# Optimization experiments

Hardware: AMD Instinct MI355X
Metric: run time of the kernel (lower is better)

The kernel has to match this reference:

```python
import jax, jax.numpy as jnp
import numpy as np

N = 100000      # nodes
E = 3200000     # edges (avg degree 32)
F = 256         # input features
C = 256         # output channels


def setup_inputs() -> dict:
    key = jax.random.key(0)
    k1, k2, k3, k4, k5 = jax.random.split(key, 5)
    x = jax.random.normal(k1, (N, F), dtype=jnp.float32)
    edge_row = jax.random.randint(k2, (E,), 0, N, dtype=jnp.int32)
    edge_col = jax.random.randint(k3, (E,), 0, N, dtype=jnp.int32)
    # precomputed normalized adjacency values (D^-1/2 (A+I) D^-1/2 entries)
    edge_vals = jax.random.uniform(k4, (E,), dtype=jnp.float32)
    kernel = jax.random.normal(k5, (F, C), dtype=jnp.float32) * (1.0 / np.sqrt(F))
    bias = jnp.zeros((C,), dtype=jnp.float32)
    return {"x": x, "edge_row": edge_row, "edge_col": edge_col,
            "edge_vals": edge_vals, "kernel": kernel, "bias": bias}


def reference(x, edge_row, edge_col, edge_vals, kernel, bias):
    # GraphConv: Z = relu( A_hat @ (X @ W) + b ), single mode, sparse A_hat.
    h = x @ kernel                                   # [N, C]
    msgs = edge_vals[:, None] * h[edge_col]          # [E, C] gather along cols
    agg = jax.ops.segment_sum(msgs, edge_row, num_segments=N)  # [N, C]
    return jax.nn.relu(agg + bias)
```

## Files before the change

kernel.cpp:

```cpp
#include <hip/hip_runtime.h>
#include <hip/hip_bf16.h>
#include <hip/hip_fp16.h>


#define BROWS 128
#define NBMAX 1024
#define CH_A1 16384
#define CH_A3 8192
#define GEMM_SMEM 10240

typedef __attribute__((ext_vector_type(4))) float f32x4;
typedef __attribute__((ext_vector_type(8))) short s16x8;

__device__ __forceinline__ unsigned short f2bf(float f) {
    unsigned u = __float_as_uint(f);
    u += 0x7FFFu + ((u >> 16) & 1u);
    return (unsigned short)(u >> 16);
}
__device__ __forceinline__ float bf2f(unsigned short s) {
    return __uint_as_float(((unsigned)s) << 16);
}

__global__ __launch_bounds__(256) void kA1h(const int* __restrict__ row,
                                            int* __restrict__ gcnt,
                                            const float* __restrict__ W,
                                            unsigned short* __restrict__ Wt,
                                            int E, int NB, int nHist) {
    __shared__ int h[NBMAX];
    int bid = blockIdx.x;
    int t = threadIdx.x;
    if (bid >= nHist) {
        int idx = (bid - nHist) * 256 + t;
        int k = idx >> 8, c = idx & 255;
        Wt[c * 256 + k] = f2bf(W[idx]);
        return;
    }
    for (int j = t; j < NB; j += 256) h[j] = 0;
    __syncthreads();
    int start = bid * CH_A1;
    int end = min(E, start + CH_A1);
    for (int i = start + t; i < end; i += 256)
        atomicAdd(&h[row[i] >> 7], 1);
    __syncthreads();
    for (int j = t; j < NB; j += 256)
        if (h[j]) atomicAdd(&gcnt[j], h[j]);
}

__global__ __launch_bounds__(1024) void kA2(const int* __restrict__ gcnt,
                                            int* __restrict__ bkt_base,
                                            int* __restrict__ gcur,
                                            int* __restrict__ rowptr,
                                            int NB, int N, int E) {
    __shared__ int s[1024];
    int t = threadIdx.x;
    int v = (t < NB) ? gcnt[t] : 0;
    s[t] = v;
    __syncthreads();
    for (int off = 1; off < 1024; off <<= 1) {
        int tmp = (t >= off) ? s[t - off] : 0;
        __syncthreads();
        if (t >= off) s[t] += tmp;
        __syncthreads();
    }
    if (t < NB) {
        int ex = s[t] - v;
        bkt_base[t] = ex;
        gcur[t] = ex;
    }
    if (t == 0) {
        bkt_base[NB] = E;
        rowptr[N] = E;
    }
}

__device__ __forceinline__ void a3_body(const int* __restrict__ row,
                                        const int* __restrict__ col,
                                        const float* __restrict__ val,
                                        int* __restrict__ gcur,
                                        int2* __restrict__ binned,
                                        int E, int NB, int chunk, char* smem) {
    int* h    = (int*)smem;
    int* base = h + NB;
    int* cur  = base + NB;
    int t = threadIdx.x;
    for (int j = t; j < NB; j += 256) { h[j] = 0; cur[j] = 0; }
    __syncthreads();
    int start = chunk * CH_A3;
    int end = min(E, start + CH_A3);
    for (int i = start + t; i < end; i += 256)
        atomicAdd(&h[row[i] >> 7], 1);
    __syncthreads();
    for (int j = t; j < NB; j += 256) {
        int c = h[j];
        base[j] = c ? atomicAdd(&gcur[j], c) : 0;
    }
    __syncthreads();
    for (int i = start + t; i < end; i += 256) {
        int r = row[i];
        int b = r >> 7;
        int ofs = atomicAdd(&cur[b], 1);
        unsigned hb = (unsigned)__half_as_ushort(__float2half(val[i]));
        binned[base[b] + ofs] = make_int2(col[i] | (int)(hb << 17), r & (BROWS - 1));
    }
}

__device__ __forceinline__ void kb_body(const int2* __restrict__ binned,
                                        const int* __restrict__ bkt_base,
                                        int* __restrict__ rowptr,
                                        unsigned* __restrict__ csr,
                                        int N, int b, char* smem) {
    int* cnt = (int*)smem;
    int* sc  = cnt + BROWS;
    int* cur = sc + BROWS;
    int t = threadIdx.x;
    int r0 = b * BROWS;
    int bb = bkt_base[b];
    int be = bkt_base[b + 1];
    if (t < BROWS) cnt[t] = 0;
    __syncthreads();
    for (int i = bb + t; i < be; i += 256)
        atomicAdd(&cnt[binned[i].y], 1);
    __syncthreads();
    if (t < BROWS) sc[t] = cnt[t];
    __syncthreads();
    for (int off = 1; off < BROWS; off <<= 1) {
        int tmp = (t < BROWS && t >= off) ? sc[t - off] : 0;
        __syncthreads();
        if (t < BROWS && t >= off) sc[t] += tmp;
        __syncthreads();
    }
    if (t < BROWS) {
        int ex = sc[t] - cnt[t];
        cur[t] = ex;
        if (r0 + t < N) rowptr[r0 + t] = bb + ex;
    }
    __syncthreads();
    for (int i = bb + t; i < be; i += 256) {
        int2 e = binned[i];
        int ofs = atomicAdd(&cur[e.y], 1);
        csr[bb + ofs] = (unsigned)e.x;
    }
}

__device__ __forceinline__ void gemm_body(const float* __restrict__ X,
                                          const unsigned short* __restrict__ Wt,
                                          unsigned short* __restrict__ H,
                                          int M, int g, char* smem) {
    typedef unsigned short AsRow[40];
    AsRow* As = (AsRow*)smem;
    int t = threadIdx.x;
    int lane = t & 63;
    int w = t >> 6;
    int wm = w & 1, wn = w >> 1;
    int rb = g >> 2, cb = g & 3;
    int r0 = rb * 128, c0 = cb * 64;

    int srow = t >> 2;
    int sslot = t & 3;
    int gr0 = r0 + srow;        if (gr0 >= M) gr0 = M - 1;
    int gr1 = r0 + 64 + srow;   if (gr1 >= M) gr1 = M - 1;

    f32x4 acc[4][2] = {};

    for (int k0 = 0; k0 < 256; k0 += 32) {
        const float* p0 = &X[(size_t)gr0 * 256 + k0 + sslot * 8];
        const float* p1 = &X[(size_t)gr1 * 256 + k0 + sslot * 8];
        float4 a0 = *(const float4*)p0;
        float4 a1 = *(const float4*)(p0 + 4);
        float4 b0 = *(const float4*)p1;
        float4 b1 = *(const float4*)(p1 + 4);
        s16x8 va, vb;
        va[0] = (short)f2bf(a0.x); va[1] = (short)f2bf(a0.y);
        va[2] = (short)f2bf(a0.z); va[3] = (short)f2bf(a0.w);
        va[4] = (short)f2bf(a1.x); va[5] = (short)f2bf(a1.y);
        va[6] = (short)f2bf(a1.z); va[7] = (short)f2bf(a1.w);
        vb[0] = (short)f2bf(b0.x); vb[1] = (short)f2bf(b0.y);
        vb[2] = (short)f2bf(b0.z); vb[3] = (short)f2bf(b0.w);
        vb[4] = (short)f2bf(b1.x); vb[5] = (short)f2bf(b1.y);
        vb[6] = (short)f2bf(b1.z); vb[7] = (short)f2bf(b1.w);
        __syncthreads();
        *(s16x8*)&As[srow][sslot * 8] = va;
        *(s16x8*)&As[srow + 64][sslot * 8] = vb;
        __syncthreads();

        int kofs = (lane >> 4) * 8;
        s16x8 afr[4], bfr[2];
#pragma unroll
        for (int mi = 0; mi < 4; ++mi)
            afr[mi] = *(const s16x8*)&As[wm * 64 + mi * 16 + (lane & 15)][kofs];
#pragma unroll
        for (int ni = 0; ni < 2; ++ni) {
            int cn = c0 + wn * 32 + ni * 16 + (lane & 15);
            bfr[ni] = *(const s16x8*)&Wt[(size_t)cn * 256 + k0 + kofs];
        }
#pragma unroll
        for (int mi = 0; mi < 4; ++mi)
#pragma unroll
            for (int ni = 0; ni < 2; ++ni)
                acc[mi][ni] = __builtin_amdgcn_mfma_f32_16x16x32_bf16(
                    afr[mi], bfr[ni], acc[mi][ni], 0, 0, 0);
    }

#pragma unroll
    for (int mi = 0; mi < 4; ++mi) {
#pragma unroll
        for (int ni = 0; ni < 2; ++ni) {
            int rg = r0 + wm * 64 + mi * 16 + (lane >> 4) * 4;
            int cg = c0 + wn * 32 + ni * 16 + (lane & 15);
#pragma unroll
            for (int j = 0; j < 4; ++j) {
                if (rg + j < M)
                    H[(size_t)(rg + j) * 256 + cg] = f2bf(acc[mi][ni][j]);
            }
        }
    }
}

__global__ __launch_bounds__(256) void hyb1(const int* __restrict__ row,
                                            const int* __restrict__ col,
                                            const float* __restrict__ val,
                                            int* __restrict__ gcur,
                                            int2* __restrict__ binned,
                                            int E, int NB, int nA3,
                                            const float* __restrict__ X,
                                            const unsigned short* __restrict__ Wt,
                                            unsigned short* __restrict__ H,
                                            int M, int g0) {
    extern __shared__ char smem[];
    int bid = blockIdx.x;
    if (bid < nA3) { a3_body(row, col, val, gcur, binned, E, NB, bid, smem); return; }
    gemm_body(X, Wt, H, M, g0 + (bid - nA3), smem);
}

__global__ __launch_bounds__(256) void hyb2(const int2* __restrict__ binned,
                                            const int* __restrict__ bktb,
                                            int* __restrict__ rowptr,
                                            unsigned* __restrict__ csr,
                                            int N, int NB,
                                            const float* __restrict__ X,
                                            const unsigned short* __restrict__ Wt,
                                            unsigned short* __restrict__ H,
                                            int M, int g0) {
    extern __shared__ char smem[];
    int bid = blockIdx.x;
    if (bid < NB) { kb_body(binned, bktb, rowptr, csr, N, bid, smem); return; }
    gemm_body(X, Wt, H, M, g0 + (bid - NB), smem);
}

__global__ __launch_bounds__(256) void k_gemm_solo(const float* __restrict__ X,
                                                   const unsigned short* __restrict__ Wt,
                                                   unsigned short* __restrict__ H, int M) {
    extern __shared__ char smem[];
    gemm_body(X, Wt, H, M, blockIdx.x, smem);
}

__global__ __launch_bounds__(256) void k_agg(const unsigned short* __restrict__ H,
                                             const int* __restrict__ rowptr,
                                             const unsigned* __restrict__ csr,
                                             const float* __restrict__ bias,
                                             float* __restrict__ out, int n) {
    int wave = threadIdx.x >> 6;
    int lane = threadIdx.x & 63;
    int node = blockIdx.x * 4 + wave;
    if (node >= n) return;
    int s = rowptr[node];
    int e = rowptr[node + 1];
    int h = lane >> 5;
    int cbase = (lane & 31) * 8;

    float a0=0.f,a1=0.f,a2=0.f,a3=0.f,a4=0.f,a5=0.f,a6=0.f,a7=0.f;

#define ACC(K, HV)                                                      \
    {                                                                   \
        float v = __half2float(__ushort_as_half((unsigned short)((K) >> 17))); \
        a0 += v * bf2f((unsigned short)(HV)[0]);                        \
        a1 += v * bf2f((unsigned short)(HV)[1]);                        \
        a2 += v * bf2f((unsigned short)(HV)[2]);                        \
        a3 += v * bf2f((unsigned short)(HV)[3]);                        \
        a4 += v * bf2f((unsigned short)(HV)[4]);                        \
        a5 += v * bf2f((unsigned short)(HV)[5]);                        \
        a6 += v * bf2f((unsigned short)(HV)[6]);                        \
        a7 += v * bf2f((unsigned short)(HV)[7]);                        \
    }

    int i = s;
    for (; i + 7 < e; i += 8) {
        unsigned k0 = csr[i + h];
        unsigned k1 = csr[i + 2 + h];
        unsigned k2 = csr[i + 4 + h];
        unsigned k3 = csr[i + 6 + h];
        s16x8 h0 = *(const s16x8*)&H[(k0 & 0x1FFFFu) * 256 + cbase];
        s16x8 h1 = *(const s16x8*)&H[(k1 & 0x1FFFFu) * 256 + cbase];
        s16x8 h2 = *(const s16x8*)&H[(k2 & 0x1FFFFu) * 256 + cbase];
        s16x8 h3 = *(const s16x8*)&H[(k3 & 0x1FFFFu) * 256 + cbase];
        ACC(k0, h0); ACC(k1, h1); ACC(k2, h2); ACC(k3, h3);
    }
    for (; i + 1 < e; i += 2) {
        unsigned k0 = csr[i + h];
        s16x8 h0 = *(const s16x8*)&H[(k0 & 0x1FFFFu) * 256 + cbase];
        ACC(k0, h0);
    }
    if (i < e) {
        unsigned k0 = csr[i];
        s16x8 h0 = *(const s16x8*)&H[(k0 & 0x1FFFFu) * 256 + cbase];
        float v = h ? 0.f
                    : __half2float(__ushort_as_half((unsigned short)(k0 >> 17)));
        a0 += v * bf2f((unsigned short)h0[0]);
        a1 += v * bf2f((unsigned short)h0[1]);
        a2 += v * bf2f((unsigned short)h0[2]);
        a3 += v * bf2f((unsigned short)h0[3]);
        a4 += v * bf2f((unsigned short)h0[4]);
        a5 += v * bf2f((unsigned short)h0[5]);
        a6 += v * bf2f((unsigned short)h0[6]);
        a7 += v * bf2f((unsigned short)h0[7]);
    }
#undef ACC

    a0 += __shfl_xor(a0, 32); a1 += __shfl_xor(a1, 32);
    a2 += __shfl_xor(a2, 32); a3 += __shfl_xor(a3, 32);
    a4 += __shfl_xor(a4, 32); a5 += __shfl_xor(a5, 32);
    a6 += __shfl_xor(a6, 32); a7 += __shfl_xor(a7, 32);

    float w0 = h ? a4 : a0;
    float w1 = h ? a5 : a1;
    float w2 = h ? a6 : a2;
    float w3 = h ? a7 : a3;
    int cw = cbase + h * 4;
    float4 b4 = *(const float4*)&bias[cw];
    float4 o;
    o.x = fmaxf(w0 + b4.x, 0.f);
    o.y = fmaxf(w1 + b4.y, 0.f);
    o.z = fmaxf(w2 + b4.z, 0.f);
    o.w = fmaxf(w3 + b4.w, 0.f);
    *(float4*)&out[node * 256 + cw] = o;
}

extern "C" void kernel_launch(void* const* d_in, const int* in_sizes, int n_in,
                              void* d_out, int out_size, void* d_ws, size_t ws_size,
                              hipStream_t stream) {
    const float* x     = (const float*)d_in[0];
    const int*   erow  = (const int*)d_in[1];
    const int*   ecol  = (const int*)d_in[2];
    const float* evals = (const float*)d_in[3];
    const float* W     = (const float*)d_in[4];
    const float* bias  = (const float*)d_in[5];
    float* out = (float*)d_out;

    const int C = 256;
    const int N = in_sizes[0] / C;
    const int E = in_sizes[1];
    const int NB = (N + BROWS - 1) / BROWS;

    char* ws = (char*)d_ws;
    size_t off = 0;
    auto carve = [&](size_t bytes) -> void* {
        void* p = ws + off;
        off += (bytes + 255) & ~(size_t)255;
        return p;
    };
    unsigned short* Hbf  = (unsigned short*)carve((size_t)N * C * 2);
    unsigned*       csr  = (unsigned*)carve((size_t)E * 4);
    int*            rowp = (int*)carve((size_t)(N + 1) * 4);
    unsigned short* Wt   = (unsigned short*)carve((size_t)C * 256 * 2);
    int*            gcnt = (int*)carve((size_t)NB * 4);
    int*            gcur = (int*)carve((size_t)NB * 4);
    int*            bktb = (int*)carve((size_t)(NB + 1) * 4);

    bool fused = (off + (size_t)E * 8) <= ws_size;
    int2* binned = fused ? (int2*)carve((size_t)E * 8) : (int2*)Hbf;

    int nHist = (E + CH_A1 - 1) / CH_A1;
    int nA3   = (E + CH_A3 - 1) / CH_A3;
    int nRB   = (N + 127) / 128;
    int gemmBlocks = nRB * 4;
    int G1 = gemmBlocks / 2;
    int G2 = gemmBlocks - G1;

    hipMemsetAsync(gcnt, 0, (size_t)NB * 4, stream);
    kA1h<<<nHist + 256, 256, 0, stream>>>(erow, gcnt, W, Wt, E, NB, nHist);
    kA2<<<1, 1024, 0, stream>>>(gcnt, bktb, gcur, rowp, NB, N, E);

    if (fused) {
        hyb1<<<nA3 + G1, 256, GEMM_SMEM, stream>>>(erow, ecol, evals, gcur, binned,
                                                   E, NB, nA3, x, Wt, Hbf, N, 0);
        hyb2<<<NB + G2, 256, GEMM_SMEM, stream>>>(binned, bktb, rowp, csr, N, NB,
                                                  x, Wt, Hbf, N, G1);
    } else {
        hyb1<<<nA3, 256, GEMM_SMEM, stream>>>(erow, ecol, evals, gcur, binned,
                                              E, NB, nA3, x, Wt, Hbf, N, 0);
        hyb2<<<NB, 256, GEMM_SMEM, stream>>>(binned, bktb, rowp, csr, N, NB,
                                             x, Wt, Hbf, N, 0);
        k_gemm_solo<<<gemmBlocks, 256, GEMM_SMEM, stream>>>(x, Wt, Hbf, N);
    }

    k_agg<<<(N + 3) / 4, 256, 0, stream>>>(Hbf, rowp, csr, bias, out, N);
}
```

Measured before the change: 435.6 us.

## Store H in 16-column blocked layout and aggregate per column block

```diff
diff --git a/kernel.cpp b/kernel.cpp
--- a/kernel.cpp
+++ b/kernel.cpp
@@ -3,7 +3,7 @@
 #include <hip/hip_fp16.h>
 
 
-#define BROWS 128
+#define BROWS 256
 #define NBMAX 1024
 #define CH_A1 16384
 #define CH_A3 8192
@@ -40,7 +40,7 @@
     int start = bid * CH_A1;
     int end = min(E, start + CH_A1);
     for (int i = start + t; i < end; i += 256)
-        atomicAdd(&h[row[i] >> 7], 1);
+        atomicAdd(&h[row[i] >> 8], 1);
     __syncthreads();
     for (int j = t; j < NB; j += 256)
         if (h[j]) atomicAdd(&gcnt[j], h[j]);
@@ -88,7 +88,7 @@
     int start = chunk * CH_A3;
     int end = min(E, start + CH_A3);
     for (int i = start + t; i < end; i += 256)
-        atomicAdd(&h[row[i] >> 7], 1);
+        atomicAdd(&h[row[i] >> 8], 1);
     __syncthreads();
     for (int j = t; j < NB; j += 256) {
         int c = h[j];
@@ -97,7 +97,7 @@
     __syncthreads();
     for (int i = start + t; i < end; i += 256) {
         int r = row[i];
-        int b = r >> 7;
+        int b = r >> 8;
         int ofs = atomicAdd(&cur[b], 1);
         unsigned hb = (unsigned)__half_as_ushort(__float2half(val[i]));
         binned[base[b] + ofs] = make_int2(col[i] | (int)(hb << 17), r & (BROWS - 1));
@@ -116,24 +116,23 @@
     int r0 = b * BROWS;
     int bb = bkt_base[b];
     int be = bkt_base[b + 1];
-    if (t < BROWS) cnt[t] = 0;
+    cnt[t] = 0;
     __syncthreads();
     for (int i = bb + t; i < be; i += 256)
         atomicAdd(&cnt[binned[i].y], 1);
     __syncthreads();
-    if (t < BROWS) sc[t] = cnt[t];
-    __syncthreads();
-    for (int off = 1; off < BROWS; off <<= 1) {
-        int tmp = (t < BROWS && t >= off) ? sc[t - off] : 0;
-        __syncthreads();
-        if (t < BROWS && t >= off) sc[t] += tmp;
-        __syncthreads();
-    }
-    if (t < BROWS) {
-        int ex = sc[t] - cnt[t];
-        cur[t] = ex;
-        if (r0 + t < N) rowptr[r0 + t] = bb + ex;
-    }
+    int v = cnt[t];
+    sc[t] = v;
+    __syncthreads();
+    for (int off = 1; off < 256; off <<= 1) {
+        int tmp = (t >= off) ? sc[t - off] : 0;
+        __syncthreads();
+        if (t >= off) sc[t] += tmp;
+        __syncthreads();
+    }
+    int ex = sc[t] - v;
+    cur[t] = ex;
+    if (r0 + t < N) rowptr[r0 + t] = bb + ex;
     __syncthreads();
     for (int i = bb + t; i < be; i += 256) {
         int2 e = binned[i];
@@ -144,7 +143,7 @@
 
 __device__ __forceinline__ void gemm_body(const float* __restrict__ X,
                                           const unsigned short* __restrict__ Wt,
-                                          unsigned short* __restrict__ H,
+                                          unsigned short* __restrict__ Hb,
                                           int M, int g, char* smem) {
     typedef unsigned short AsRow[40];
     AsRow* As = (AsRow*)smem;
@@ -152,8 +151,8 @@
     int lane = t & 63;
     int w = t >> 6;
     int wm = w & 1, wn = w >> 1;
-    int rb = g >> 2, cb = g & 3;
-    int r0 = rb * 128, c0 = cb * 64;
+    int rb = g >> 2, cb4 = g & 3;
+    int r0 = rb * 128, c0 = cb4 * 64;
 
     int srow = t >> 2;
     int sslot = t & 3;
@@ -207,10 +206,12 @@
         for (int ni = 0; ni < 2; ++ni) {
             int rg = r0 + wm * 64 + mi * 16 + (lane >> 4) * 4;
             int cg = c0 + wn * 32 + ni * 16 + (lane & 15);
+            int cbk = cg >> 4;
+            int cw  = cg & 15;
 #pragma unroll
             for (int j = 0; j < 4; ++j) {
                 if (rg + j < M)
-                    H[(size_t)(rg + j) * 256 + cg] = f2bf(acc[mi][ni][j]);
+                    Hb[((size_t)cbk * M + (rg + j)) * 16 + cw] = f2bf(acc[mi][ni][j]);
             }
         }
     }
@@ -224,12 +225,12 @@
                                             int E, int NB, int nA3,
                                             const float* __restrict__ X,
                                             const unsigned short* __restrict__ Wt,
-                                            unsigned short* __restrict__ H,
+                                            unsigned short* __restrict__ Hb,
                                             int M, int g0) {
     extern __shared__ char smem[];
     int bid = blockIdx.x;
     if (bid < nA3) { a3_body(row, col, val, gcur, binned, E, NB, bid, smem); return; }
-    gemm_body(X, Wt, H, M, g0 + (bid - nA3), smem);
+    gemm_body(X, Wt, Hb, M, g0 + (bid - nA3), smem);
 }
 
 __global__ __launch_bounds__(256) void hyb2(const int2* __restrict__ binned,
@@ -239,100 +240,75 @@
                                             int N, int NB,
                                             const float* __restrict__ X,
                                             const unsigned short* __restrict__ Wt,
-                                            unsigned short* __restrict__ H,
+                                            unsigned short* __restrict__ Hb,
                                             int M, int g0) {
     extern __shared__ char smem[];
     int bid = blockIdx.x;
     if (bid < NB) { kb_body(binned, bktb, rowptr, csr, N, bid, smem); return; }
-    gemm_body(X, Wt, H, M, g0 + (bid - NB), smem);
+    gemm_body(X, Wt, Hb, M, g0 + (bid - NB), smem);
 }
 
 __global__ __launch_bounds__(256) void k_gemm_solo(const float* __restrict__ X,
                                                    const unsigned short* __restrict__ Wt,
-                                                   unsigned short* __restrict__ H, int M) {
+                                                   unsigned short* __restrict__ Hb, int M) {
     extern __shared__ char smem[];
-    gemm_body(X, Wt, H, M, blockIdx.x, smem);
-}
-
-__global__ __launch_bounds__(256) void k_agg(const unsigned short* __restrict__ H,
+    gemm_body(X, Wt, Hb, M, blockIdx.x, smem);
+}
+
+__global__ __launch_bounds__(256) void k_agg(const unsigned short* __restrict__ Hb,
                                              const int* __restrict__ rowptr,
                                              const unsigned* __restrict__ csr,
                                              const float* __restrict__ bias,
-                                             float* __restrict__ out, int n) {
-    int wave = threadIdx.x >> 6;
-    int lane = threadIdx.x & 63;
-    int node = blockIdx.x * 4 + wave;
-    if (node >= n) return;
-    int s = rowptr[node];
-    int e = rowptr[node + 1];
-    int h = lane >> 5;
-    int cbase = (lane & 31) * 8;
-
-    float a0=0.f,a1=0.f,a2=0.f,a3=0.f,a4=0.f,a5=0.f,a6=0.f,a7=0.f;
-
-#define ACC(K, HV)                                                      \
-    {                                                                   \
-        float v = __half2float(__ushort_as_half((unsigned short)((K) >> 17))); \
-        a0 += v * bf2f((unsigned short)(HV)[0]);                        \
-        a1 += v * bf2f((unsigned short)(HV)[1]);                        \
-        a2 += v * bf2f((unsigned short)(HV)[2]);                        \
-        a3 += v * bf2f((unsigned short)(HV)[3]);                        \
-        a4 += v * bf2f((unsigned short)(HV)[4]);                        \
-        a5 += v * bf2f((unsigned short)(HV)[5]);                        \
-        a6 += v * bf2f((unsigned short)(HV)[6]);                        \
-        a7 += v * bf2f((unsigned short)(HV)[7]);                        \
-    }
+                                             float* __restrict__ out,
+                                             int N, int PBLK) {
+    int b = blockIdx.x;
+    int phase = (b >= 8 * PBLK) ? 1 : 0;
+    int bb = b - phase * 8 * PBLK;
+    int cb = 2 * (bb & 7) + phase;
+    int nblk = bb >> 3;
+    int t = threadIdx.x;
+    int wave = t >> 6, lane = t & 63;
+    int g = lane >> 2;
+    int slot = lane & 3;
+    int node = (nblk * 4 + wave) * 16 + g;
+    const unsigned short* Hc = Hb + (size_t)cb * N * 16;
+
+    int s = 0, e = 0;
+    if (node < N) { s = rowptr[node]; e = rowptr[node + 1]; }
+
+    float a0 = 0.f, a1 = 0.f, a2 = 0.f, a3 = 0.f;
 
     int i = s;
-    for (; i + 7 < e; i += 8) {
-        unsigned k0 = csr[i + h];
-        unsigned k1 = csr[i + 2 + h];
-        unsigned k2 = csr[i + 4 + h];
-        unsigned k3 = csr[i + 6 + h];
-        s16x8 h0 = *(const s16x8*)&H[(k0 & 0x1FFFFu) * 256 + cbase];
-        s16x8 h1 = *(const s16x8*)&H[(k1 & 0x1FFFFu) * 256 + cbase];
-        s16x8 h2 = *(const s16x8*)&H[(k2 & 0x1FFFFu) * 256 + cbase];
-        s16x8 h3 = *(const s16x8*)&H[(k3 & 0x1FFFFu) * 256 + cbase];
-        ACC(k0, h0); ACC(k1, h1); ACC(k2, h2); ACC(k3, h3);
-    }
     for (; i + 1 < e; i += 2) {
-        unsigned k0 = csr[i + h];
-        s16x8 h0 = *(const s16x8*)&H[(k0 & 0x1FFFFu) * 256 + cbase];
-        ACC(k0, h0);
+        unsigned k0 = csr[i];
+        unsigned k1 = csr[i + 1];
+        ushort4 h0 = *(const ushort4*)&Hc[(size_t)(k0 & 0x1FFFFu) * 16 + slot * 4];
+        ushort4 h1 = *(const ushort4*)&Hc[(size_t)(k1 & 0x1FFFFu) * 16 + slot * 4];
+        float v0 = __half2float(__ushort_as_half((unsigned short)(k0 >> 17)));
+        float v1 = __half2float(__ushort_as_half((unsigned short)(k1 >> 17)));
+        a0 += v0 * bf2f(h0.x); a1 += v0 * bf2f(h0.y);
+        a2 += v0 * bf2f(h0.z); a3 += v0 * bf2f(h0.w);
+        a0 += v1 * bf2f(h1.x); a1 += v1 * bf2f(h1.y);
+        a2 += v1 * bf2f(h1.z); a3 += v1 * bf2f(h1.w);
     }
     if (i < e) {
         unsigned k0 = csr[i];
-        s16x8 h0 = *(const s16x8*)&H[(k0 & 0x1FFFFu) * 256 + cbase];
-        float v = h ? 0.f
-                    : __half2float(__ushort_as_half((unsigned short)(k0 >> 17)));
-        a0 += v * bf2f((unsigned short)h0[0]);
-        a1 += v * bf2f((unsigned short)h0[1]);
-        a2 += v * bf2f((unsigned short)h0[2]);
-        a3 += v * bf2f((unsigned short)h0[3]);
-        a4 += v * bf2f((unsigned short)h0[4]);
-        a5 += v * bf2f((unsigned short)h0[5]);
-        a6 += v * bf2f((unsigned short)h0[6]);
-        a7 += v * bf2f((unsigned short)h0[7]);
-    }
-#undef ACC
-
-    a0 += __shfl_xor(a0, 32); a1 += __shfl_xor(a1, 32);
-    a2 += __shfl_xor(a2, 32); a3 += __shfl_xor(a3, 32);
-    a4 += __shfl_xor(a4, 32); a5 += __shfl_xor(a5, 32);
-    a6 += __shfl_xor(a6, 32); a7 += __shfl_xor(a7, 32);
-
-    float w0 = h ? a4 : a0;
-    float w1 = h ? a5 : a1;
-    float w2 = h ? a6 : a2;
-    float w3 = h ? a7 : a3;
-    int cw = cbase + h * 4;
-    float4 b4 = *(const float4*)&bias[cw];
-    float4 o;
-    o.x = fmaxf(w0 + b4.x, 0.f);
-    o.y = fmaxf(w1 + b4.y, 0.f);
-    o.z = fmaxf(w2 + b4.z, 0.f);
-    o.w = fmaxf(w3 + b4.w, 0.f);
-    *(float4*)&out[node * 256 + cw] = o;
+        ushort4 h0 = *(const ushort4*)&Hc[(size_t)(k0 & 0x1FFFFu) * 16 + slot * 4];
+        float v0 = __half2float(__ushort_as_half((unsigned short)(k0 >> 17)));
+        a0 += v0 * bf2f(h0.x); a1 += v0 * bf2f(h0.y);
+        a2 += v0 * bf2f(h0.z); a3 += v0 * bf2f(h0.w);
+    }
+
+    if (node < N) {
+        int cw = cb * 16 + slot * 4;
+        float4 b4 = *(const float4*)&bias[cw];
+        float4 o;
+        o.x = fmaxf(a0 + b4.x, 0.f);
+        o.y = fmaxf(a1 + b4.y, 0.f);
+        o.z = fmaxf(a2 + b4.z, 0.f);
+        o.w = fmaxf(a3 + b4.w, 0.f);
+        *(float4*)&out[(size_t)node * 256 + cw] = o;
+    }
 }
 
 extern "C" void kernel_launch(void* const* d_in, const int* in_sizes, int n_in,
@@ -393,5 +369,6 @@
         k_gemm_solo<<<gemmBlocks, 256, GEMM_SMEM, stream>>>(x, Wt, Hbf, N);
     }
 
-    k_agg<<<(N + 3) / 4, 256, 0, stream>>>(Hbf, rowp, csr, bias, out, N);
-}
+    int PBLK = (N + 63) / 64;
+    k_agg<<<16 * PBLK, 256, 0, stream>>>(Hbf, rowp, csr, bias, out, N, PBLK);
+}
```

Result: slower. 624.7 us (+43.4%).

## Overlap GEMM with histogram pass and deepen aggregation gather unroll

Applied to the files above, without the earlier changes.

```diff
diff --git a/kernel.cpp b/kernel.cpp
--- a/kernel.cpp
+++ b/kernel.cpp
@@ -4,7 +4,6 @@
 
 
 #define BROWS 128
-#define NBMAX 1024
 #define CH_A1 16384
 #define CH_A3 8192
 #define GEMM_SMEM 10240
@@ -21,125 +20,11 @@
     return __uint_as_float(((unsigned)s) << 16);
 }
 
-__global__ __launch_bounds__(256) void kA1h(const int* __restrict__ row,
-                                            int* __restrict__ gcnt,
-                                            const float* __restrict__ W,
-                                            unsigned short* __restrict__ Wt,
-                                            int E, int NB, int nHist) {
-    __shared__ int h[NBMAX];
-    int bid = blockIdx.x;
-    int t = threadIdx.x;
-    if (bid >= nHist) {
-        int idx = (bid - nHist) * 256 + t;
-        int k = idx >> 8, c = idx & 255;
-        Wt[c * 256 + k] = f2bf(W[idx]);
-        return;
-    }
-    for (int j = t; j < NB; j += 256) h[j] = 0;
-    __syncthreads();
-    int start = bid * CH_A1;
-    int end = min(E, start + CH_A1);
-    for (int i = start + t; i < end; i += 256)
-        atomicAdd(&h[row[i] >> 7], 1);
-    __syncthreads();
-    for (int j = t; j < NB; j += 256)
-        if (h[j]) atomicAdd(&gcnt[j], h[j]);
-}
-
-__global__ __launch_bounds__(1024) void kA2(const int* __restrict__ gcnt,
-                                            int* __restrict__ bkt_base,
-                                            int* __restrict__ gcur,
-                                            int* __restrict__ rowptr,
-                                            int NB, int N, int E) {
-    __shared__ int s[1024];
-    int t = threadIdx.x;
-    int v = (t < NB) ? gcnt[t] : 0;
-    s[t] = v;
-    __syncthreads();
-    for (int off = 1; off < 1024; off <<= 1) {
-        int tmp = (t >= off) ? s[t - off] : 0;
-        __syncthreads();
-        if (t >= off) s[t] += tmp;
-        __syncthreads();
-    }
-    if (t < NB) {
-        int ex = s[t] - v;
-        bkt_base[t] = ex;
-        gcur[t] = ex;
-    }
-    if (t == 0) {
-        bkt_base[NB] = E;
-        rowptr[N] = E;
-    }
-}
-
-__device__ __forceinline__ void a3_body(const int* __restrict__ row,
-                                        const int* __restrict__ col,
-                                        const float* __restrict__ val,
-                                        int* __restrict__ gcur,
-                                        int2* __restrict__ binned,
-                                        int E, int NB, int chunk, char* smem) {
-    int* h    = (int*)smem;
-    int* base = h + NB;
-    int* cur  = base + NB;
-    int t = threadIdx.x;
-    for (int j = t; j < NB; j += 256) { h[j] = 0; cur[j] = 0; }
-    __syncthreads();
-    int start = chunk * CH_A3;
-    int end = min(E, start + CH_A3);
-    for (int i = start + t; i < end; i += 256)
-        atomicAdd(&h[row[i] >> 7], 1);
-    __syncthreads();
-    for (int j = t; j < NB; j += 256) {
-        int c = h[j];
-        base[j] = c ? atomicAdd(&gcur[j], c) : 0;
-    }
-    __syncthreads();
-    for (int i = start + t; i < end; i += 256) {
-        int r = row[i];
-        int b = r >> 7;
-        int ofs = atomicAdd(&cur[b], 1);
-        unsigned hb = (unsigned)__half_as_ushort(__float2half(val[i]));
-        binned[base[b] + ofs] = make_int2(col[i] | (int)(hb << 17), r & (BROWS - 1));
-    }
-}
-
-__device__ __forceinline__ void kb_body(const int2* __restrict__ binned,
-                                        const int* __restrict__ bkt_base,
-                                        int* __restrict__ rowptr,
-                                        unsigned* __restrict__ csr,
-                                        int N, int b, char* smem) {
-    int* cnt = (int*)smem;
-    int* sc  = cnt + BROWS;
-    int* cur = sc + BROWS;
-    int t = threadIdx.x;
-    int r0 = b * BROWS;
-    int bb = bkt_base[b];
-    int be = bkt_base[b + 1];
-    if (t < BROWS) cnt[t] = 0;
-    __syncthreads();
-    for (int i = bb + t; i < be; i += 256)
-        atomicAdd(&cnt[binned[i].y], 1);
-    __syncthreads();
-    if (t < BROWS) sc[t] = cnt[t];
-    __syncthreads();
-    for (int off = 1; off < BROWS; off <<= 1) {
-        int tmp = (t < BROWS && t >= off) ? sc[t - off] : 0;
-        __syncthreads();
-        if (t < BROWS && t >= off) sc[t] += tmp;
-        __syncthreads();
-    }
-    if (t < BROWS) {
-        int ex = sc[t] - cnt[t];
-        cur[t] = ex;
-        if (r0 + t < N) rowptr[r0 + t] = bb + ex;
-    }
-    __syncthreads();
-    for (int i = bb + t; i < be; i += 256) {
-        int2 e = binned[i];
-        int ofs = atomicAdd(&cur[e.y], 1);
-        csr[bb + ofs] = (unsigned)e.x;
-    }
+__global__ __launch_bounds__(256) void k_wt(const float* __restrict__ W,
+                                            unsigned short* __restrict__ Wt) {
+    int idx = blockIdx.x * 256 + threadIdx.x;
+    int k = idx >> 8, c = idx & 255;
+    Wt[c * 256 + k] = f2bf(W[idx]);
 }
 
 __device__ __forceinline__ void gemm_body(const float* __restrict__ X,
@@ -152,8 +37,8 @@
     int lane = t & 63;
     int w = t >> 6;
     int wm = w & 1, wn = w >> 1;
-    int rb = g >> 2, cb = g & 3;
-    int r0 = rb * 128, c0 = cb * 64;
+    int rb = g >> 2, cb4 = g & 3;
+    int r0 = rb * 128, c0 = cb4 * 64;
 
     int srow = t >> 2;
     int sslot = t & 3;
@@ -216,31 +101,156 @@
     }
 }
 
-__global__ __launch_bounds__(256) void hyb1(const int* __restrict__ row,
-                                            const int* __restrict__ col,
-                                            const float* __restrict__ val,
+__device__ __forceinline__ void hist_body(const int* __restrict__ row,
+                                          int* __restrict__ gcnt,
+                                          int E, int NB, int chunk, char* smem) {
+    int* h = (int*)smem;
+    int t = threadIdx.x;
+    for (int j = t; j < NB; j += 256) h[j] = 0;
+    __syncthreads();
+    int start = chunk * CH_A1;
+    int end = min(E, start + CH_A1);
+    for (int i = start + t; i < end; i += 256)
+        atomicAdd(&h[row[i] >> 7], 1);
+    __syncthreads();
+    for (int j = t; j < NB; j += 256)
+        if (h[j]) atomicAdd(&gcnt[j], h[j]);
+}
+
+__device__ __forceinline__ void a3_body(const int* __restrict__ row,
+                                        const int* __restrict__ col,
+                                        const float* __restrict__ val,
+                                        int* __restrict__ gcur,
+                                        int2* __restrict__ binned,
+                                        int E, int NB, int chunk, char* smem) {
+    int* h    = (int*)smem;
+    int* base = h + NB;
+    int* cur  = base + NB;
+    int t = threadIdx.x;
+    for (int j = t; j < NB; j += 256) { h[j] = 0; cur[j] = 0; }
+    __syncthreads();
+    int start = chunk * CH_A3;
+    int end = min(E, start + CH_A3);
+    for (int i = start + t; i < end; i += 256)
+        atomicAdd(&h[row[i] >> 7], 1);
+    __syncthreads();
+    for (int j = t; j < NB; j += 256) {
+        int c = h[j];
+        base[j] = c ? atomicAdd(&gcur[j], c) : 0;
+    }
+    __syncthreads();
+    for (int i = start + t; i < end; i += 256) {
+        int r = row[i];
+        int b = r >> 7;
+        int ofs = atomicAdd(&cur[b], 1);
+        unsigned hb = (unsigned)__half_as_ushort(__float2half(val[i]));
+        binned[base[b] + ofs] = make_int2(col[i] | (int)(hb << 17), r & (BROWS - 1));
+    }
+}
+
+__device__ __forceinline__ void kb_body(const int2* __restrict__ binned,
+                                        const int* __restrict__ bkt_base,
+                                        int* __restrict__ rowptr,
+                                        unsigned* __restrict__ csr,
+                                        int N, int b, char* smem) {
+    int* cnt = (int*)smem;
+    int* sc  = cnt + BROWS;
+    int* cur = sc + BROWS;
+    int t = threadIdx.x;
+    int r0 = b * BROWS;
+    int bb = bkt_base[b];
+    int be = bkt_base[b + 1];
+    if (t < BROWS) cnt[t] = 0;
+    __syncthreads();
+    for (int i = bb + t; i < be; i += 256)
+        atomicAdd(&cnt[binned[i].y], 1);
+    __syncthreads();
+    if (t < BROWS) sc[t] = cnt[t];
+    __syncthreads();
+    for (int off = 1; off < BROWS; off <<= 1) {
+        int tmp = (t < BROWS && t >= off) ? sc[t - off] : 0;
+        __syncthreads();
+        if (t < BROWS && t >= off) sc[t] += tmp;
+        __syncthreads();
+    }
+    if (t < BROWS) {
+        int ex = sc[t] - cnt[t];
+        cur[t] = ex;
+        if (r0 + t < N) rowptr[r0 + t] = bb + ex;
+    }
+    __syncthreads();
+    for (int i = bb + t; i < be; i += 256) {
+        int2 e = binned[i];
+        int ofs = atomicAdd(&cur[e.y], 1);
+        csr[bb + ofs] = (unsigned)e.x;
+    }
+}
+
+__global__ __launch_bounds__(1024) void kA2(const int* __restrict__ gcnt,
+                                            int* __restrict__ bkt_base,
                                             int* __restrict__ gcur,
-                                            int2* __restrict__ binned,
-                                            int E, int NB, int nA3,
-                                            const float* __restrict__ X,
-                                            const unsigned short* __restrict__ Wt,
-                                            unsigned short* __restrict__ H,
-                                            int M, int g0) {
+                                            int* __restrict__ rowptr,
+                                            int NB, int N, int E) {
+    __shared__ int s[1024];
+    int t = threadIdx.x;
+    int v = (t < NB) ? gcnt[t] : 0;
+    s[t] = v;
+    __syncthreads();
+    for (int off = 1; off < 1024; off <<= 1) {
+        int tmp = (t >= off) ? s[t - off] : 0;
+        __syncthreads();
+        if (t >= off) s[t] += tmp;
+        __syncthreads();
+    }
+    if (t < NB) {
+        int ex = s[t] - v;
+        bkt_base[t] = ex;
+        gcur[t] = ex;
+    }
+    if (t == 0) {
+        bkt_base[NB] = E;
+        rowptr[N] = E;
+    }
+}
+
+__global__ __launch_bounds__(256) void h0(const int* __restrict__ row,
+                                          int* __restrict__ gcnt,
+                                          int E, int NB, int nHist,
+                                          const float* __restrict__ X,
+                                          const unsigned short* __restrict__ Wt,
+                                          unsigned short* __restrict__ H,
+                                          int M, int g0) {
+    extern __shared__ char smem[];
+    int bid = blockIdx.x;
+    if (bid < nHist) { hist_body(row, gcnt, E, NB, bid, smem); return; }
+    gemm_body(X, Wt, H, M, g0 + (bid - nHist), smem);
+}
+
+__global__ __launch_bounds__(256) void h1(const int* __restrict__ row,
+                                          const int* __restrict__ col,
+                                          const float* __restrict__ val,
+                                          int* __restrict__ gcur,
+                                          int2* __restrict__ binned,
+                                          int E, int NB, int nA3,
+                                          const float* __restrict__ X,
+                                          const unsigned short* __restrict__ Wt,
+                                          unsigned short* __restrict__ H,
+                                          int M, int g0) {
     extern __shared__ char smem[];
     int bid = blockIdx.x;
     if (bid < nA3) { a3_body(row, col, val, gcur, binned, E, NB, bid, smem); return; }
     gemm_body(X, Wt, H, M, g0 + (bid - nA3), smem);
 }
 
-__global__ __launch_bounds__(256) void hyb2(const int2* __restrict__ binned,
-                                            const int* __restrict__ bktb,
-                                            int* __restrict__ rowptr,
-                                            unsigned* __restrict__ csr,
-                                            int N, int NB,
-                                            const float* __restrict__ X,
-                                            const unsigned short* __restrict__ Wt,
-                                            unsigned short* __restrict__ H,
-                                            int M, int g0) {
+__global__ __launch_bounds__(256) void h2(const int2* __restrict__ binned,
+                                          const int* __restrict__ bktb,
+                                          int* __restrict__ rowptr,
+                                          unsigned* __restrict__ csr,
+                                          int N, int NB,
+                                          const float* __restrict__ X,
+                                          const unsigned short* __restrict__ Wt,
+                                          unsigned short* __restrict__ H,
+                                          int M, int g0) {
     extern __shared__ char smem[];
     int bid = blockIdx.x;
     if (bid < NB) { kb_body(binned, bktb, rowptr, csr, N, bid, smem); return; }
@@ -284,35 +294,47 @@
     }
 
     int i = s;
-    for (; i + 7 < e; i += 8) {
+    for (; i + 11 < e; i += 12) {
         unsigned k0 = csr[i + h];
         unsigned k1 = csr[i + 2 + h];
         unsigned k2 = csr[i + 4 + h];
         unsigned k3 = csr[i + 6 + h];
-        s16x8 h0 = *(const s16x8*)&H[(k0 & 0x1FFFFu) * 256 + cbase];
-        s16x8 h1 = *(const s16x8*)&H[(k1 & 0x1FFFFu) * 256 + cbase];
-        s16x8 h2 = *(const s16x8*)&H[(k2 & 0x1FFFFu) * 256 + cbase];
-        s16x8 h3 = *(const s16x8*)&H[(k3 & 0x1FFFFu) * 256 + cbase];
-        ACC(k0, h0); ACC(k1, h1); ACC(k2, h2); ACC(k3, h3);
+        unsigned k4 = csr[i + 8 + h];
+        unsigned k5 = csr[i + 10 + h];
+        s16x8 g0 = *(const s16x8*)&H[(k0 & 0x1FFFFu) * 256 + cbase];
+        s16x8 g1 = *(const s16x8*)&H[(k1 & 0x1FFFFu) * 256 + cbase];
+        s16x8 g2 = *(const s16x8*)&H[(k2 & 0x1FFFFu) * 256 + cbase];
+        s16x8 g3 = *(const s16x8*)&H[(k3 & 0x1FFFFu) * 256 + cbase];
+        s16x8 g4 = *(const s16x8*)&H[(k4 & 0x1FFFFu) * 256 + cbase];
+        s16x8 g5 = *(const s16x8*)&H[(k5 & 0x1FFFFu) * 256 + cbase];
+        ACC(k0, g0); ACC(k1, g1); ACC(k2, g2);
+        ACC(k3, g3); ACC(k4, g4); ACC(k5, g5);
+    }
+    for (; i + 3 < e; i += 4) {
+        unsigned k0 = csr[i + h];
+        unsigned k1 = csr[i + 2 + h];
+        s16x8 g0 = *(const s16x8*)&H[(k0 & 0x1FFFFu) * 256 + cbase];
+        s16x8 g1 = *(const s16x8*)&H[(k1 & 0x1FFFFu) * 256 + cbase];
+        ACC(k0, g0); ACC(k1, g1);
     }
     for (; i + 1 < e; i += 2) {
         unsigned k0 = csr[i + h];
-        s16x8 h0 = *(const s16x8*)&H[(k0 & 0x1FFFFu) * 256 + cbase];
-        ACC(k0, h0);
+        s16x8 g0 = *(const s16x8*)&H[(k0 & 0x1FFFFu) * 256 + cbase];
+        ACC(k0, g0);
     }
     if (i < e) {
         unsigned k0 = csr[i];
-        s16x8 h0 = *(const s16x8*)&H[(k0 & 0x1FFFFu) * 256 + cbase];
+        s16x8 g0 = *(const s16x8*)&H[(k0 & 0x1FFFFu) * 256 + cbase];
         float v = h ? 0.f
                     : __half2float(__ushort_as_half((unsigned short)(k0 >> 17)));
-        a0 += v * bf2f((unsigned short)h0[0]);
-        a1 += v * bf2f((unsigned short)h0[1]);
-        a2 += v * bf2f((unsigned short)h0[2]);
-        a3 += v * bf2f((unsigned short)h0[3]);
-        a4 += v * bf2f((unsigned short)h0[4]);
-        a5 += v * bf2f((unsigned short)h0[5]);
-        a6 += v * bf2f((unsigned short)h0[6]);
-        a7 += v * bf2f((unsigned short)h0[7]);
+        a0 += v * bf2f((unsigned short)g0[0]);
+        a1 += v * bf2f((unsigned short)g0[1]);
+        a2 += v * bf2f((unsigned short)g0[2]);
+        a3 += v * bf2f((unsigned short)g0[3]);
+        a4 += v * bf2f((unsigned short)g0[4]);
+        a5 += v * bf2f((unsigned short)g0[5]);
+        a6 += v * bf2f((unsigned short)g0[6]);
+        a7 += v * bf2f((unsigned short)g0[7]);
     }
 #undef ACC
 
@@ -371,27 +393,23 @@
 
     int nHist = (E + CH_A1 - 1) / CH_A1;
     int nA3   = (E + CH_A3 - 1) / CH_A3;
-    int nRB   = (N + 127) / 128;
-    int gemmBlocks = nRB * 4;
-    int G1 = gemmBlocks / 2;
-    int G2 = gemmBlocks - G1;
+    int gemmBlocks = ((N + 127) / 128) * 4;
+
+    int G0 = fused ? 600 : 0;
+    int G1 = fused ? 1400 : 0;
+    int G2 = fused ? (gemmBlocks - 600 - 1400) : 0;
 
     hipMemsetAsync(gcnt, 0, (size_t)NB * 4, stream);
-    kA1h<<<nHist + 256, 256, 0, stream>>>(erow, gcnt, W, Wt, E, NB, nHist);
+    k_wt<<<256, 256, 0, stream>>>(W, Wt);
+    h0<<<nHist + G0, 256, GEMM_SMEM, stream>>>(erow, gcnt, E, NB, nHist,
+                                               x, Wt, Hbf, N, 0);
     kA2<<<1, 1024, 0, stream>>>(gcnt, bktb, gcur, rowp, NB, N, E);
-
-    if (fused) {
-        hyb1<<<nA3 + G1, 256, GEMM_SMEM, stream>>>(erow, ecol, evals, gcur, binned,
-                                                   E, NB, nA3, x, Wt, Hbf, N, 0);
-        hyb2<<<NB + G2, 256, GEMM_SMEM, stream>>>(binned, bktb, rowp, csr, N, NB,
-                                                  x, Wt, Hbf, N, G1);
-    } else {
-        hyb1<<<nA3, 256, GEMM_SMEM, stream>>>(erow, ecol, evals, gcur, binned,
-                                              E, NB, nA3, x, Wt, Hbf, N, 0);
-        hyb2<<<NB, 256, GEMM_SMEM, stream>>>(binned, bktb, rowp, csr, N, NB,
-                                             x, Wt, Hbf, N, 0);
+    h1<<<nA3 + G1, 256, GEMM_SMEM, stream>>>(erow, ecol, evals, gcur, binned,
+                                             E, NB, nA3, x, Wt, Hbf, N, G0);
+    h2<<<NB + G2, 256, GEMM_SMEM, stream>>>(binned, bktb, rowp, csr, N, NB,
+                                            x, Wt, Hbf, N, G0 + G1);
+    if (!fused)
         k_gemm_solo<<<gemmBlocks, 256, GEMM_SMEM, stream>>>(x, Wt, Hbf, N);
-    }
 
     k_agg<<<(N + 3) / 4, 256, 0, stream>>>(Hbf, rowp, csr, bias, out, N);
 }
```

After: 432.0 us. About the same (-0.8%).
